# Optimization experiments

Hardware: AMD Instinct MI355X
Metric: run time of the kernel (lower is better)

The kernel has to match this reference:

```python
import jax, jax.numpy as jnp
import numpy as np

EMB = 1024
CTX = 32
F_IN, R, F_OUT = 1024, 16, 1024
N_EXP = 16
H1 = 2048   # expert / gating hidden
H2 = 512    # expert output width
B = 8


def _init(key, shape, fan_in):
    return jax.random.normal(key, shape, dtype=jnp.float32) / np.sqrt(fan_in)


def setup_inputs() -> dict:
    key = jax.random.key(0)
    ks = jax.random.split(key, 14)
    return {
        "s": jax.random.normal(ks[0], (B, EMB), dtype=jnp.float32),
        # gating: Linear(EMB,2048) -> ReLU -> Linear(2048,N_EXP) -> Softmax
        "Wg1": _init(ks[1], (EMB, H1), EMB),
        "bg1": jnp.zeros((H1,), jnp.float32),
        "Wg2": _init(ks[2], (H1, N_EXP), H1),
        "bg2": jnp.zeros((N_EXP,), jnp.float32),
        # experts (stacked): Linear(EMB+CTX,2048) -> ReLU -> Linear(2048,512)
        "W1": _init(ks[3], (N_EXP, EMB + CTX, H1), EMB + CTX),
        "b1": jnp.zeros((N_EXP, H1), jnp.float32),
        "W2": _init(ks[4], (N_EXP, H1, H2), H1),
        "b2": jnp.zeros((N_EXP, H2), jnp.float32),
        # decoders
        "WA": _init(ks[5], (H2, F_IN * R), H2),
        "bA": jnp.zeros((F_IN * R,), jnp.float32),
        "WB": _init(ks[6], (H2, R * F_OUT), H2),
        "bB": jnp.zeros((R * F_OUT,), jnp.float32),
    }


def reference(s, Wg1, bg1, Wg2, bg2, W1, b1, W2, b2, WA, bA, WB, bB):
    # gating weights over experts: [B, E]
    weights = jax.nn.softmax(jax.nn.relu(s @ Wg1 + bg1) @ Wg2 + bg2, axis=-1)

    # Expert layer-1. Input is concat([s, one_hot(c)]); since the context part
    # is a one-hot, its contribution is just a row of the context block of W1.
    W1s = W1[:, :EMB, :]              # [E, EMB, H1]
    W1c = W1[:, EMB:, :]              # [E, CTX, H1]
    base = jnp.einsum('bi,eih->ebh', s, W1s) + b1[:, None, :]   # [E, B, H1]
    # h[c,e,b,:] = relu(base[e,b,:] + W1c[e,c,:])
    h = jax.nn.relu(base[None] + jnp.transpose(W1c, (1, 0, 2))[:, :, None, :])  # [C,E,B,H1]

    # Expert layer-2: [C, E, B, H2]
    eo = jnp.einsum('cebh,ehd->cebd', h, W2) + b2[None, :, None, :]

    # softmax-weighted mixture over experts: [C, B, H2]
    z = jnp.einsum('be,cebd->cbd', weights, eo)

    A = (z @ WA + bA).reshape(CTX, B, F_IN, R)
    Bm = (z @ WB + bB).reshape(CTX, B, R, F_OUT)
    return A, Bm
```

## Files before the change

kernel.cpp:

```cpp
#include <hip/hip_runtime.h>
#include <hip/hip_bf16.h>

#define EMB 1024
#define CTX 32
#define NEXP 16
#define H1 2048
#define H2 512
#define NBIG 16384

typedef __attribute__((ext_vector_type(8))) short short8;
typedef __attribute__((ext_vector_type(4))) float floatx4;
typedef const __attribute__((address_space(1))) void* gas_t;
typedef __attribute__((address_space(3))) void* las_t;

__device__ __forceinline__ void gl16(const unsigned short* g, unsigned short* l) {
  __builtin_amdgcn_global_load_lds((gas_t)(const void*)g, (las_t)(void*)l, 16, 0, 0);
}

__device__ inline unsigned short bf_bits(float x) {
  unsigned u = __builtin_bit_cast(unsigned, x);
  u += 0x7fffu + ((u >> 16) & 1u);
  return (unsigned short)(u >> 16);
}
__device__ inline unsigned pk_bf16(float a, float b) {
  return (unsigned)bf_bits(a) | ((unsigned)bf_bits(b) << 16);
}

__global__ void __launch_bounds__(256) k_gate1(const float* __restrict__ s,
                                               const float* __restrict__ Wg1,
                                               const float* __restrict__ bg1,
                                               float* __restrict__ g1) {
  __shared__ float red[16][16][8];
  int t = threadIdx.x;
  int c = t & 15, kk = t >> 4;
  int h = blockIdx.x * 16 + c;
  float acc[8];
#pragma unroll
  for (int b = 0; b < 8; ++b) acc[b] = 0.f;
  int k0 = kk * 64;
  for (int k = k0; k < k0 + 64; ++k) {
    float w = Wg1[(size_t)k * H1 + h];
#pragma unroll
    for (int b = 0; b < 8; ++b) acc[b] += s[b * EMB + k] * w;
  }
#pragma unroll
  for (int b = 0; b < 8; ++b) red[kk][c][b] = acc[b];
  __syncthreads();
  if (t < 128) {
    int cc = t >> 3, b = t & 7;
    float v = 0.f;
#pragma unroll
    for (int q = 0; q < 16; ++q) v += red[q][cc][b];
    int hh = blockIdx.x * 16 + cc;
    v += bg1[hh];
    g1[b * H1 + hh] = fmaxf(v, 0.f);
  }
}

__global__ void __launch_bounds__(256) k_gate2(const float* __restrict__ g1,
                                               const float* __restrict__ Wg2,
                                               const float* __restrict__ bg2,
                                               float* __restrict__ logits) {
  __shared__ float red[256][8];
  int e = blockIdx.x, t = threadIdx.x;
  int k0 = t * 8;
  float wv[8];
#pragma unroll
  for (int j = 0; j < 8; ++j) wv[j] = Wg2[(size_t)(k0 + j) * NEXP + e];
  float acc[8];
#pragma unroll
  for (int b = 0; b < 8; ++b) {
    float4 ga = *(const float4*)&g1[b * H1 + k0];
    float4 gb = *(const float4*)&g1[b * H1 + k0 + 4];
    acc[b] = ga.x * wv[0] + ga.y * wv[1] + ga.z * wv[2] + ga.w * wv[3] +
             gb.x * wv[4] + gb.y * wv[5] + gb.z * wv[6] + gb.w * wv[7];
  }
#pragma unroll
  for (int b = 0; b < 8; ++b) red[t][b] = acc[b];
  __syncthreads();
  for (int off = 128; off > 0; off >>= 1) {
    if (t < off) {
#pragma unroll
      for (int b = 0; b < 8; ++b) red[t][b] += red[t + off][b];
    }
    __syncthreads();
  }
  if (t < 8) logits[t * NEXP + e] = red[0][t] + bg2[e];
}

__global__ void __launch_bounds__(512) k_base(const float* __restrict__ s,
                                              const float* __restrict__ W1,
                                              const float* __restrict__ b1,
                                              float* __restrict__ base) {
  __shared__ float sl[8 * EMB];
  __shared__ float red[8][64][17];
  int t = threadIdx.x;
  int ht = blockIdx.x;
  int e = blockIdx.y;
#pragma unroll
  for (int i = 0; i < 4; ++i) {
    int idx = (t + i * 512) * 4;
    *(float4*)&sl[idx] = *(const float4*)&s[idx];
  }
  __syncthreads();
  int hp = t & 63;
  int kk = t >> 6;
  int h = ht * 128 + hp * 2;
  const float* wp = W1 + (size_t)e * 1056 * H1 + h;
  float a0[8], a1[8];
#pragma unroll
  for (int b = 0; b < 8; ++b) { a0[b] = 0.f; a1[b] = 0.f; }
  int k0 = kk * 128;
  for (int k = k0; k < k0 + 128; ++k) {
    float2 w = *(const float2*)(wp + (size_t)k * H1);
#pragma unroll
    for (int b = 0; b < 8; ++b) {
      float sv = sl[b * EMB + k];
      a0[b] += sv * w.x;
      a1[b] += sv * w.y;
    }
  }
#pragma unroll
  for (int b = 0; b < 8; ++b) {
    red[kk][hp][b * 2] = a0[b];
    red[kk][hp][b * 2 + 1] = a1[b];
  }
  __syncthreads();
  if (t < 64) {
    int hh = ht * 128 + t * 2;
#pragma unroll
    for (int b = 0; b < 8; ++b) {
      float v0 = 0.f, v1 = 0.f;
#pragma unroll
      for (int q = 0; q < 8; ++q) {
        v0 += red[q][t][b * 2];
        v1 += red[q][t][b * 2 + 1];
      }
      float2 bv = *(const float2*)&b1[e * H1 + hh];
      float2 o;
      o.x = v0 + bv.x;
      o.y = v1 + bv.y;
      *(float2*)&base[(size_t)(e * 8 + b) * H1 + hh] = o;
    }
  }
}

__global__ void __launch_bounds__(256) k_packW(const float* __restrict__ src,
                                               unsigned short* __restrict__ dst,
                                               int Nsrc, int Ndst, int n_off,
                                               long sbs, long dbs) {
  __shared__ float tl[64][65];
  int nt = blockIdx.x, kb = blockIdx.y, bz = blockIdx.z, t = threadIdx.x;
  const float* S = src + (size_t)bz * sbs + (size_t)kb * 64 * Nsrc + nt * 64;
  int r = t >> 4, c4 = (t & 15) * 4;
#pragma unroll
  for (int i = 0; i < 4; ++i) {
    int row = r + i * 16;
    float4 v = *(const float4*)&S[(size_t)row * Nsrc + c4];
    *(float4*)&tl[row][c4] = v;
  }
  __syncthreads();
  int nl = t >> 2;
  int cb = (t & 3) * 2;
  int key = nl & 7;
  unsigned short* D = dst + (size_t)bz * dbs +
                      ((size_t)kb * Ndst + n_off + nt * 64 + nl) * 64;
#pragma unroll
  for (int j = 0; j < 2; ++j) {
    int cp = cb + j;
    int k0 = (cp ^ key) * 8;
    union { short8 v; unsigned u[4]; } p;
#pragma unroll
    for (int q = 0; q < 4; ++q)
      p.u[q] = pk_bf16(tl[k0 + 2 * q][nl], tl[k0 + 2 * q + 1][nl]);
    *(short8*)&D[cp * 8] = p.v;
  }
}

__global__ void __launch_bounds__(512) k_egemm2(const float* __restrict__ base,
                                                const float* __restrict__ W1,
                                                const unsigned short* __restrict__ W2t,
                                                float* __restrict__ eo2) {
  __shared__ __align__(16) unsigned short As[4096];
  __shared__ __align__(16) unsigned short Bs[16384];
  int id = blockIdx.x;
  int mt = id >> 6, rem = id & 63;
  int e = rem >> 2, nt = (rem >> 1) & 1, ks = rem & 1;
  int t = threadIdx.x, lane = t & 63, w = t >> 6;
  int wm = w >> 2, wn = w & 3;
  int fr = lane & 15, quad = lane >> 4, key = fr & 7;

  int am = t >> 3;
  int ak = (t & 7) * 8;
  const float* bp = base + ((size_t)e * 8 + (am & 7)) * H1;
  const float* cp = W1 + ((size_t)e * 1056 + EMB + mt * 8 + (am >> 3)) * H1;
  unsigned short* adst = &As[am * 64 + (((t & 7) ^ (am & 7)) * 8)];
  const unsigned short* wBe = W2t + (size_t)e * 1048576 + (size_t)nt * 16384;

  floatx4 zero4 = {0.f, 0.f, 0.f, 0.f};
  floatx4 acc[2][4];
#pragma unroll
  for (int i = 0; i < 2; ++i)
#pragma unroll
    for (int j = 0; j < 4; ++j) acc[i][j] = zero4;

  for (int i = 0; i < 16; ++i) {
    int kb = ks * 16 + i;
    __syncthreads();
    const unsigned short* bsrc = wBe + (size_t)kb * 32768 + t * 8;
    gl16(bsrc, &Bs[t * 8]);
    gl16(bsrc + 4096, &Bs[t * 8 + 4096]);
    gl16(bsrc + 8192, &Bs[t * 8 + 8192]);
    gl16(bsrc + 12288, &Bs[t * 8 + 12288]);
    int k0 = kb * 64 + ak;
    float4 x0 = *(const float4*)&bp[k0];
    float4 x1 = *(const float4*)&bp[k0 + 4];
    float4 y0 = *(const float4*)&cp[k0];
    float4 y1 = *(const float4*)&cp[k0 + 4];
    union { short8 v; unsigned u[4]; } pq;
    pq.u[0] = pk_bf16(fmaxf(x0.x + y0.x, 0.f), fmaxf(x0.y + y0.y, 0.f));
    pq.u[1] = pk_bf16(fmaxf(x0.z + y0.z, 0.f), fmaxf(x0.w + y0.w, 0.f));
    pq.u[2] = pk_bf16(fmaxf(x1.x + y1.x, 0.f), fmaxf(x1.y + y1.y, 0.f));
    pq.u[3] = pk_bf16(fmaxf(x1.z + y1.z, 0.f), fmaxf(x1.w + y1.w, 0.f));
    *(short8*)adst = pq.v;
    __syncthreads();
#pragma unroll
    for (int ks2 = 0; ks2 < 2; ++ks2) {
      int cof = ((ks2 * 4 + quad) ^ key) * 8;
      short8 a0 = *(const short8*)&As[(wm * 32 + fr) * 64 + cof];
      short8 a1 = *(const short8*)&As[(wm * 32 + 16 + fr) * 64 + cof];
#pragma unroll
      for (int nj = 0; nj < 4; ++nj) {
        short8 bf = *(const short8*)&Bs[(wn * 64 + nj * 16 + fr) * 64 + cof];
        acc[0][nj] = __builtin_amdgcn_mfma_f32_16x16x32_bf16(a0, bf, acc[0][nj], 0, 0, 0);
        acc[1][nj] = __builtin_amdgcn_mfma_f32_16x16x32_bf16(a1, bf, acc[1][nj], 0, 0, 0);
      }
    }
  }
  float* op = eo2 + (size_t)ks * 2097152;
  int d0 = nt * 256 + wn * 64 + fr;
#pragma unroll
  for (int nj = 0; nj < 4; ++nj) {
    int d = d0 + nj * 16;
#pragma unroll
    for (int rt = 0; rt < 2; ++rt) {
#pragma unroll
      for (int i2 = 0; i2 < 4; ++i2) {
        int gm = mt * 64 + wm * 32 + rt * 16 + quad * 4 + i2;
        op[(((size_t)(gm >> 3) * NEXP + e) * 8 + (gm & 7)) * H2 + d] = acc[rt][nj][i2];
      }
    }
  }
}

__global__ void __launch_bounds__(256) k_mix(const float* __restrict__ eo2,
                                             const float* __restrict__ logits,
                                             const float* __restrict__ b2,
                                             unsigned short* __restrict__ z_t) {
  int c = blockIdx.x, half = blockIdx.y, t = threadIdx.x;
  int b = t >> 5;
  int dc = half * 32 + (t & 31);
  int d0 = dc * 8;
  int m = c * 8 + b;
  float lg[16];
  float mx = -1e30f;
#pragma unroll
  for (int e = 0; e < 16; ++e) {
    lg[e] = logits[b * NEXP + e];
    mx = fmaxf(mx, lg[e]);
  }
  float sum = 0.f;
#pragma unroll
  for (int e = 0; e < 16; ++e) {
    lg[e] = __expf(lg[e] - mx);
    sum += lg[e];
  }
  float inv = 1.f / sum;
  float o[8];
#pragma unroll
  for (int j = 0; j < 8; ++j) o[j] = 0.f;
#pragma unroll
  for (int e = 0; e < 16; ++e) {
    float wl = lg[e] * inv;
    const float* p = &eo2[(((size_t)c * NEXP + e) * 8 + b) * H2 + d0];
    float4 x0 = *(const float4*)p;
    float4 x1 = *(const float4*)(p + 4);
    float4 y0 = *(const float4*)(p + 2097152);
    float4 y1 = *(const float4*)(p + 2097152 + 4);
    float4 v0 = *(const float4*)&b2[e * H2 + d0];
    float4 v1 = *(const float4*)&b2[e * H2 + d0 + 4];
    o[0] += wl * (x0.x + y0.x + v0.x);
    o[1] += wl * (x0.y + y0.y + v0.y);
    o[2] += wl * (x0.z + y0.z + v0.z);
    o[3] += wl * (x0.w + y0.w + v0.w);
    o[4] += wl * (x1.x + y1.x + v1.x);
    o[5] += wl * (x1.y + y1.y + v1.y);
    o[6] += wl * (x1.z + y1.z + v1.z);
    o[7] += wl * (x1.w + y1.w + v1.w);
  }
  union { short8 v; unsigned u[4]; } p;
#pragma unroll
  for (int q = 0; q < 4; ++q) p.u[q] = pk_bf16(o[2 * q], o[2 * q + 1]);
  int kb = dc >> 3;
  int cpx = (dc & 7) ^ (b & 7);
  *(short8*)&z_t[((size_t)kb * 256 + m) * 64 + cpx * 8] = p.v;
}

__global__ void __launch_bounds__(512) k_lora2(const unsigned short* __restrict__ z_t,
                                               const float* __restrict__ WA,
                                               const float* __restrict__ WB,
                                               const float* __restrict__ bA,
                                               const float* __restrict__ bB,
                                               float* __restrict__ out) {
  __shared__ __align__(16) unsigned short As[16384];
  __shared__ __align__(16) unsigned short Bs[8192];
  int nt = blockIdx.x;
  int t = threadIdx.x, lane = t & 63, w = t >> 6;
  int wm = w >> 1, wn = w & 1;
  int fr = lane & 15, quad = lane >> 4, key = fr & 7;
  int ms = nt >> 7;
  const float* Wsrc = ms ? WB : WA;
  int col0 = (nt & 127) * 128;
  int bn = t & 127, kg = t >> 7;
  const float* bw = Wsrc + col0 + bn;
  unsigned short* bd0 = &Bs[bn * 64 + (((kg * 2) ^ (bn & 7)) * 8)];
  unsigned short* bd1 = &Bs[bn * 64 + (((kg * 2 + 1) ^ (bn & 7)) * 8)];

  floatx4 zero4 = {0.f, 0.f, 0.f, 0.f};
  floatx4 acc[4][4];
#pragma unroll
  for (int i = 0; i < 4; ++i)
#pragma unroll
    for (int j = 0; j < 4; ++j) acc[i][j] = zero4;

  for (int kb = 0; kb < 8; ++kb) {
    __syncthreads();
    const unsigned short* asrc = z_t + (size_t)kb * 16384 + t * 8;
    gl16(asrc, &As[t * 8]);
    gl16(asrc + 4096, &As[t * 8 + 4096]);
    gl16(asrc + 8192, &As[t * 8 + 8192]);
    gl16(asrc + 12288, &As[t * 8 + 12288]);
    const float* bk = bw + (size_t)(kb * 64 + kg * 16) * NBIG;
    float v[16];
#pragma unroll
    for (int kr = 0; kr < 16; ++kr) v[kr] = bk[(size_t)kr * NBIG];
    union { short8 s; unsigned u[4]; } q0, q1;
#pragma unroll
    for (int q = 0; q < 4; ++q) {
      q0.u[q] = pk_bf16(v[2 * q], v[2 * q + 1]);
      q1.u[q] = pk_bf16(v[8 + 2 * q], v[9 + 2 * q]);
    }
    *(short8*)bd0 = q0.s;
    *(short8*)bd1 = q1.s;
    __syncthreads();
#pragma unroll
    for (int ks2 = 0; ks2 < 2; ++ks2) {
      int cof = ((ks2 * 4 + quad) ^ key) * 8;
      short8 bf0 = *(const short8*)&Bs[(wn * 64 + fr) * 64 + cof];
      short8 bf1 = *(const short8*)&Bs[(wn * 64 + 16 + fr) * 64 + cof];
      short8 bf2 = *(const short8*)&Bs[(wn * 64 + 32 + fr) * 64 + cof];
      short8 bf3 = *(const short8*)&Bs[(wn * 64 + 48 + fr) * 64 + cof];
#pragma unroll
      for (int rt = 0; rt < 4; ++rt) {
        short8 af = *(const short8*)&As[(wm * 64 + rt * 16 + fr) * 64 + cof];
        acc[rt][0] = __builtin_amdgcn_mfma_f32_16x16x32_bf16(af, bf0, acc[rt][0], 0, 0, 0);
        acc[rt][1] = __builtin_amdgcn_mfma_f32_16x16x32_bf16(af, bf1, acc[rt][1], 0, 0, 0);
        acc[rt][2] = __builtin_amdgcn_mfma_f32_16x16x32_bf16(af, bf2, acc[rt][2], 0, 0, 0);
        acc[rt][3] = __builtin_amdgcn_mfma_f32_16x16x32_bf16(af, bf3, acc[rt][3], 0, 0, 0);
      }
    }
  }
  const float* bias = ms ? bB : bA;
  float* obase = out + (size_t)ms * 4194304;
#pragma unroll
  for (int nj = 0; nj < 4; ++nj) {
    int nn = col0 + wn * 64 + nj * 16 + fr;
    float bv = bias[nn];
#pragma unroll
    for (int rt = 0; rt < 4; ++rt) {
#pragma unroll
      for (int i2 = 0; i2 < 4; ++i2) {
        int m = wm * 64 + rt * 16 + quad * 4 + i2;
        obase[(size_t)m * NBIG + nn] = acc[rt][nj][i2] + bv;
      }
    }
  }
}

extern "C" void kernel_launch(void* const* d_in, const int* in_sizes, int n_in,
                              void* d_out, int out_size, void* d_ws, size_t ws_size,
                              hipStream_t stream) {
  const float* s = (const float*)d_in[0];
  const float* Wg1 = (const float*)d_in[1];
  const float* bg1 = (const float*)d_in[2];
  const float* Wg2 = (const float*)d_in[3];
  const float* bg2 = (const float*)d_in[4];
  const float* W1 = (const float*)d_in[5];
  const float* b1 = (const float*)d_in[6];
  const float* W2 = (const float*)d_in[7];
  const float* b2 = (const float*)d_in[8];
  const float* WA = (const float*)d_in[9];
  const float* bA = (const float*)d_in[10];
  const float* WB = (const float*)d_in[11];
  const float* bB = (const float*)d_in[12];
  float* out = (float*)d_out;

  char* ws = (char*)d_ws;
  float* g1 = (float*)(ws);
  float* logits = (float*)(ws + 65536);
  float* base = (float*)(ws + 131072);
  float* eo2 = (float*)(ws + 1179648);
  unsigned short* z_t = (unsigned short*)(ws + 17956864);
  unsigned short* W2t = (unsigned short*)(ws + 18219008);

  k_gate1<<<128, 256, 0, stream>>>(s, Wg1, bg1, g1);
  k_gate2<<<16, 256, 0, stream>>>(g1, Wg2, bg2, logits);
  k_base<<<dim3(16, 16), 512, 0, stream>>>(s, W1, b1, base);
  k_packW<<<dim3(8, 32, 16), 256, 0, stream>>>(W2, W2t, H2, H2, 0,
                                               (long)H1 * H2, (long)H1 * H2);
  k_egemm2<<<256, 512, 0, stream>>>(base, W1, W2t, eo2);
  k_mix<<<dim3(32, 2), 256, 0, stream>>>(eo2, logits, b2, z_t);
  k_lora2<<<256, 512, 0, stream>>>(z_t, WA, WB, bA, bB, out);
}
```

Before: 390.0 us.

## Merge independent pre-stage kernels into two heterogeneous launches and widen mix grid

Gate layer 1, the expert base GEMV and the W2 bf16 repack are merged into one launch whose block ID picks the role. Gate layer 2 is folded into the expert GEMM launch as extra blocks. The mix kernel's grid is doubled with each thread handling four outputs instead of eight. This cuts launch count and lets independent work overlap on idle CUs. In exchange, the fused kernel carries a large shared allocation (about 66 KB) for every block, which may lower occupancy for the many small repack blocks.

```diff
diff --git a/kernel.cpp b/kernel.cpp
--- a/kernel.cpp
+++ b/kernel.cpp
@@ -10,6 +10,7 @@
 
 typedef __attribute__((ext_vector_type(8))) short short8;
 typedef __attribute__((ext_vector_type(4))) float floatx4;
+typedef __attribute__((ext_vector_type(2))) unsigned uint2v;
 typedef const __attribute__((address_space(1))) void* gas_t;
 typedef __attribute__((address_space(3))) void* las_t;
 
@@ -26,230 +27,230 @@
   return (unsigned)bf_bits(a) | ((unsigned)bf_bits(b) << 16);
 }
 
-__global__ void __launch_bounds__(256) k_gate1(const float* __restrict__ s,
-                                               const float* __restrict__ Wg1,
-                                               const float* __restrict__ bg1,
-                                               float* __restrict__ g1) {
-  __shared__ float red[16][16][8];
+__global__ void __launch_bounds__(512) k_fusedA(const float* __restrict__ s,
+                                                const float* __restrict__ Wg1,
+                                                const float* __restrict__ bg1,
+                                                const float* __restrict__ W1,
+                                                const float* __restrict__ b1,
+                                                const float* __restrict__ W2,
+                                                float* __restrict__ g1,
+                                                float* __restrict__ base,
+                                                unsigned short* __restrict__ W2t) {
+  __shared__ __align__(16) char smem[67584];
+  int bid = blockIdx.x;
   int t = threadIdx.x;
-  int c = t & 15, kk = t >> 4;
-  int h = blockIdx.x * 16 + c;
-  float acc[8];
-#pragma unroll
-  for (int b = 0; b < 8; ++b) acc[b] = 0.f;
-  int k0 = kk * 64;
-  for (int k = k0; k < k0 + 64; ++k) {
-    float w = Wg1[(size_t)k * H1 + h];
-#pragma unroll
-    for (int b = 0; b < 8; ++b) acc[b] += s[b * EMB + k] * w;
-  }
-#pragma unroll
-  for (int b = 0; b < 8; ++b) red[kk][c][b] = acc[b];
-  __syncthreads();
-  if (t < 128) {
-    int cc = t >> 3, b = t & 7;
-    float v = 0.f;
-#pragma unroll
-    for (int q = 0; q < 16; ++q) v += red[q][cc][b];
-    int hh = blockIdx.x * 16 + cc;
-    v += bg1[hh];
-    g1[b * H1 + hh] = fmaxf(v, 0.f);
-  }
-}
-
-__global__ void __launch_bounds__(256) k_gate2(const float* __restrict__ g1,
-                                               const float* __restrict__ Wg2,
-                                               const float* __restrict__ bg2,
-                                               float* __restrict__ logits) {
-  __shared__ float red[256][8];
-  int e = blockIdx.x, t = threadIdx.x;
-  int k0 = t * 8;
-  float wv[8];
-#pragma unroll
-  for (int j = 0; j < 8; ++j) wv[j] = Wg2[(size_t)(k0 + j) * NEXP + e];
-  float acc[8];
-#pragma unroll
-  for (int b = 0; b < 8; ++b) {
-    float4 ga = *(const float4*)&g1[b * H1 + k0];
-    float4 gb = *(const float4*)&g1[b * H1 + k0 + 4];
-    acc[b] = ga.x * wv[0] + ga.y * wv[1] + ga.z * wv[2] + ga.w * wv[3] +
-             gb.x * wv[4] + gb.y * wv[5] + gb.z * wv[6] + gb.w * wv[7];
-  }
-#pragma unroll
-  for (int b = 0; b < 8; ++b) red[t][b] = acc[b];
-  __syncthreads();
-  for (int off = 128; off > 0; off >>= 1) {
-    if (t < off) {
-#pragma unroll
-      for (int b = 0; b < 8; ++b) red[t][b] += red[t + off][b];
-    }
-    __syncthreads();
-  }
-  if (t < 8) logits[t * NEXP + e] = red[0][t] + bg2[e];
-}
-
-__global__ void __launch_bounds__(512) k_base(const float* __restrict__ s,
-                                              const float* __restrict__ W1,
-                                              const float* __restrict__ b1,
-                                              float* __restrict__ base) {
-  __shared__ float sl[8 * EMB];
-  __shared__ float red[8][64][17];
-  int t = threadIdx.x;
-  int ht = blockIdx.x;
-  int e = blockIdx.y;
-#pragma unroll
-  for (int i = 0; i < 4; ++i) {
-    int idx = (t + i * 512) * 4;
-    *(float4*)&sl[idx] = *(const float4*)&s[idx];
-  }
-  __syncthreads();
-  int hp = t & 63;
-  int kk = t >> 6;
-  int h = ht * 128 + hp * 2;
-  const float* wp = W1 + (size_t)e * 1056 * H1 + h;
-  float a0[8], a1[8];
-#pragma unroll
-  for (int b = 0; b < 8; ++b) { a0[b] = 0.f; a1[b] = 0.f; }
-  int k0 = kk * 128;
-  for (int k = k0; k < k0 + 128; ++k) {
-    float2 w = *(const float2*)(wp + (size_t)k * H1);
+
+  if (bid < 256) {
+    float* sl = (float*)smem;
+    float(*red)[64][17] = (float(*)[64][17])(smem + 32768);
+    int ht = bid & 15;
+    int e = bid >> 4;
+#pragma unroll
+    for (int i = 0; i < 4; ++i) {
+      int idx = (t + i * 512) * 4;
+      *(float4*)&sl[idx] = *(const float4*)&s[idx];
+    }
+    __syncthreads();
+    int hp = t & 63;
+    int kk = t >> 6;
+    int h = ht * 128 + hp * 2;
+    const float* wp = W1 + (size_t)e * 1056 * H1 + h;
+    float a0[8], a1[8];
+#pragma unroll
+    for (int b = 0; b < 8; ++b) { a0[b] = 0.f; a1[b] = 0.f; }
+    int k0 = kk * 128;
+    for (int k = k0; k < k0 + 128; ++k) {
+      float2 w = *(const float2*)(wp + (size_t)k * H1);
+#pragma unroll
+      for (int b = 0; b < 8; ++b) {
+        float sv = sl[b * EMB + k];
+        a0[b] += sv * w.x;
+        a1[b] += sv * w.y;
+      }
+    }
 #pragma unroll
     for (int b = 0; b < 8; ++b) {
-      float sv = sl[b * EMB + k];
-      a0[b] += sv * w.x;
-      a1[b] += sv * w.y;
-    }
-  }
-#pragma unroll
-  for (int b = 0; b < 8; ++b) {
-    red[kk][hp][b * 2] = a0[b];
-    red[kk][hp][b * 2 + 1] = a1[b];
-  }
-  __syncthreads();
-  if (t < 64) {
-    int hh = ht * 128 + t * 2;
-#pragma unroll
-    for (int b = 0; b < 8; ++b) {
-      float v0 = 0.f, v1 = 0.f;
-#pragma unroll
-      for (int q = 0; q < 8; ++q) {
-        v0 += red[q][t][b * 2];
-        v1 += red[q][t][b * 2 + 1];
-      }
-      float2 bv = *(const float2*)&b1[e * H1 + hh];
-      float2 o;
-      o.x = v0 + bv.x;
-      o.y = v1 + bv.y;
-      *(float2*)&base[(size_t)(e * 8 + b) * H1 + hh] = o;
-    }
-  }
-}
-
-__global__ void __launch_bounds__(256) k_packW(const float* __restrict__ src,
-                                               unsigned short* __restrict__ dst,
-                                               int Nsrc, int Ndst, int n_off,
-                                               long sbs, long dbs) {
-  __shared__ float tl[64][65];
-  int nt = blockIdx.x, kb = blockIdx.y, bz = blockIdx.z, t = threadIdx.x;
-  const float* S = src + (size_t)bz * sbs + (size_t)kb * 64 * Nsrc + nt * 64;
-  int r = t >> 4, c4 = (t & 15) * 4;
-#pragma unroll
-  for (int i = 0; i < 4; ++i) {
-    int row = r + i * 16;
-    float4 v = *(const float4*)&S[(size_t)row * Nsrc + c4];
-    *(float4*)&tl[row][c4] = v;
-  }
-  __syncthreads();
-  int nl = t >> 2;
-  int cb = (t & 3) * 2;
-  int key = nl & 7;
-  unsigned short* D = dst + (size_t)bz * dbs +
-                      ((size_t)kb * Ndst + n_off + nt * 64 + nl) * 64;
-#pragma unroll
-  for (int j = 0; j < 2; ++j) {
-    int cp = cb + j;
+      red[kk][hp][b * 2] = a0[b];
+      red[kk][hp][b * 2 + 1] = a1[b];
+    }
+    __syncthreads();
+    if (t < 64) {
+      int hh = ht * 128 + t * 2;
+#pragma unroll
+      for (int b = 0; b < 8; ++b) {
+        float v0 = 0.f, v1 = 0.f;
+#pragma unroll
+        for (int q = 0; q < 8; ++q) {
+          v0 += red[q][t][b * 2];
+          v1 += red[q][t][b * 2 + 1];
+        }
+        float2 bv = *(const float2*)&b1[e * H1 + hh];
+        float2 o;
+        o.x = v0 + bv.x;
+        o.y = v1 + bv.y;
+        *(float2*)&base[(size_t)(e * 8 + b) * H1 + hh] = o;
+      }
+    }
+  } else if (bid < 4352) {
+    float(*tl)[65] = (float(*)[65])smem;
+    int pid = bid - 256;
+    int nt = pid & 7, kb = (pid >> 3) & 31, e = pid >> 8;
+    const float* S = W2 + (size_t)e * H1 * H2 + (size_t)kb * 64 * H2 + nt * 64;
+    int r = t >> 4, c4 = (t & 15) * 4;
+#pragma unroll
+    for (int i = 0; i < 2; ++i) {
+      int row = r + i * 32;
+      float4 v = *(const float4*)&S[(size_t)row * H2 + c4];
+      *(float4*)&tl[row][c4] = v;
+    }
+    __syncthreads();
+    int nl = t >> 3;
+    int cp = t & 7;
+    int key = nl & 7;
+    unsigned short* D = W2t + (size_t)e * 1048576 +
+                        ((size_t)kb * 512 + nt * 64 + nl) * 64;
     int k0 = (cp ^ key) * 8;
     union { short8 v; unsigned u[4]; } p;
 #pragma unroll
     for (int q = 0; q < 4; ++q)
       p.u[q] = pk_bf16(tl[k0 + 2 * q][nl], tl[k0 + 2 * q + 1][nl]);
     *(short8*)&D[cp * 8] = p.v;
-  }
-}
-
-__global__ void __launch_bounds__(512) k_egemm2(const float* __restrict__ base,
+  } else {
+    float(*red1)[16][8] = (float(*)[16][8])smem;
+    int gid = bid - 4352;
+    int c = t & 15, kk = t >> 4;
+    int h = gid * 16 + c;
+    float acc[8];
+#pragma unroll
+    for (int b = 0; b < 8; ++b) acc[b] = 0.f;
+    int k0 = kk * 32;
+    for (int k = k0; k < k0 + 32; ++k) {
+      float w = Wg1[(size_t)k * H1 + h];
+#pragma unroll
+      for (int b = 0; b < 8; ++b) acc[b] += s[b * EMB + k] * w;
+    }
+#pragma unroll
+    for (int b = 0; b < 8; ++b) red1[kk][c][b] = acc[b];
+    __syncthreads();
+    if (t < 128) {
+      int cc = t >> 3, b = t & 7;
+      float v = 0.f;
+#pragma unroll
+      for (int q = 0; q < 32; ++q) v += red1[q][cc][b];
+      int hh = gid * 16 + cc;
+      v += bg1[hh];
+      g1[b * H1 + hh] = fmaxf(v, 0.f);
+    }
+  }
+}
+
+__global__ void __launch_bounds__(512) k_fusedB(const float* __restrict__ base,
                                                 const float* __restrict__ W1,
                                                 const unsigned short* __restrict__ W2t,
-                                                float* __restrict__ eo2) {
-  __shared__ __align__(16) unsigned short As[4096];
-  __shared__ __align__(16) unsigned short Bs[16384];
-  int id = blockIdx.x;
-  int mt = id >> 6, rem = id & 63;
-  int e = rem >> 2, nt = (rem >> 1) & 1, ks = rem & 1;
-  int t = threadIdx.x, lane = t & 63, w = t >> 6;
-  int wm = w >> 2, wn = w & 3;
-  int fr = lane & 15, quad = lane >> 4, key = fr & 7;
-
-  int am = t >> 3;
-  int ak = (t & 7) * 8;
-  const float* bp = base + ((size_t)e * 8 + (am & 7)) * H1;
-  const float* cp = W1 + ((size_t)e * 1056 + EMB + mt * 8 + (am >> 3)) * H1;
-  unsigned short* adst = &As[am * 64 + (((t & 7) ^ (am & 7)) * 8)];
-  const unsigned short* wBe = W2t + (size_t)e * 1048576 + (size_t)nt * 16384;
-
-  floatx4 zero4 = {0.f, 0.f, 0.f, 0.f};
-  floatx4 acc[2][4];
-#pragma unroll
-  for (int i = 0; i < 2; ++i)
-#pragma unroll
-    for (int j = 0; j < 4; ++j) acc[i][j] = zero4;
-
-  for (int i = 0; i < 16; ++i) {
-    int kb = ks * 16 + i;
-    __syncthreads();
-    const unsigned short* bsrc = wBe + (size_t)kb * 32768 + t * 8;
-    gl16(bsrc, &Bs[t * 8]);
-    gl16(bsrc + 4096, &Bs[t * 8 + 4096]);
-    gl16(bsrc + 8192, &Bs[t * 8 + 8192]);
-    gl16(bsrc + 12288, &Bs[t * 8 + 12288]);
-    int k0 = kb * 64 + ak;
-    float4 x0 = *(const float4*)&bp[k0];
-    float4 x1 = *(const float4*)&bp[k0 + 4];
-    float4 y0 = *(const float4*)&cp[k0];
-    float4 y1 = *(const float4*)&cp[k0 + 4];
-    union { short8 v; unsigned u[4]; } pq;
-    pq.u[0] = pk_bf16(fmaxf(x0.x + y0.x, 0.f), fmaxf(x0.y + y0.y, 0.f));
-    pq.u[1] = pk_bf16(fmaxf(x0.z + y0.z, 0.f), fmaxf(x0.w + y0.w, 0.f));
-    pq.u[2] = pk_bf16(fmaxf(x1.x + y1.x, 0.f), fmaxf(x1.y + y1.y, 0.f));
-    pq.u[3] = pk_bf16(fmaxf(x1.z + y1.z, 0.f), fmaxf(x1.w + y1.w, 0.f));
-    *(short8*)adst = pq.v;
-    __syncthreads();
-#pragma unroll
-    for (int ks2 = 0; ks2 < 2; ++ks2) {
-      int cof = ((ks2 * 4 + quad) ^ key) * 8;
-      short8 a0 = *(const short8*)&As[(wm * 32 + fr) * 64 + cof];
-      short8 a1 = *(const short8*)&As[(wm * 32 + 16 + fr) * 64 + cof];
-#pragma unroll
-      for (int nj = 0; nj < 4; ++nj) {
-        short8 bf = *(const short8*)&Bs[(wn * 64 + nj * 16 + fr) * 64 + cof];
-        acc[0][nj] = __builtin_amdgcn_mfma_f32_16x16x32_bf16(a0, bf, acc[0][nj], 0, 0, 0);
-        acc[1][nj] = __builtin_amdgcn_mfma_f32_16x16x32_bf16(a1, bf, acc[1][nj], 0, 0, 0);
-      }
-    }
-  }
-  float* op = eo2 + (size_t)ks * 2097152;
-  int d0 = nt * 256 + wn * 64 + fr;
-#pragma unroll
-  for (int nj = 0; nj < 4; ++nj) {
-    int d = d0 + nj * 16;
-#pragma unroll
-    for (int rt = 0; rt < 2; ++rt) {
-#pragma unroll
-      for (int i2 = 0; i2 < 4; ++i2) {
-        int gm = mt * 64 + wm * 32 + rt * 16 + quad * 4 + i2;
-        op[(((size_t)(gm >> 3) * NEXP + e) * 8 + (gm & 7)) * H2 + d] = acc[rt][nj][i2];
-      }
-    }
+                                                const float* __restrict__ g1,
+                                                const float* __restrict__ Wg2,
+                                                const float* __restrict__ bg2,
+                                                float* __restrict__ eo2,
+                                                float* __restrict__ logits) {
+  __shared__ __align__(16) char smemB[40960];
+  int bid = blockIdx.x;
+  int t = threadIdx.x;
+
+  if (bid < 256) {
+    unsigned short* As = (unsigned short*)smemB;
+    unsigned short* Bs = (unsigned short*)(smemB + 8192);
+    int id = bid;
+    int mt = id >> 6, rem = id & 63;
+    int e = rem >> 2, nt = (rem >> 1) & 1, ks = rem & 1;
+    int lane = t & 63, w = t >> 6;
+    int wm = w >> 2, wn = w & 3;
+    int fr = lane & 15, quad = lane >> 4, key = fr & 7;
+
+    int am = t >> 3;
+    int ak = (t & 7) * 8;
+    const float* bp = base + ((size_t)e * 8 + (am & 7)) * H1;
+    const float* cp = W1 + ((size_t)e * 1056 + EMB + mt * 8 + (am >> 3)) * H1;
+    unsigned short* adst = &As[am * 64 + (((t & 7) ^ (am & 7)) * 8)];
+    const unsigned short* wBe = W2t + (size_t)e * 1048576 + (size_t)nt * 16384;
+
+    floatx4 zero4 = {0.f, 0.f, 0.f, 0.f};
+    floatx4 acc[2][4];
+#pragma unroll
+    for (int i = 0; i < 2; ++i)
+#pragma unroll
+      for (int j = 0; j < 4; ++j) acc[i][j] = zero4;
+
+    for (int i = 0; i < 16; ++i) {
+      int kb = ks * 16 + i;
+      __syncthreads();
+      const unsigned short* bsrc = wBe + (size_t)kb * 32768 + t * 8;
+      gl16(bsrc, &Bs[t * 8]);
+      gl16(bsrc + 4096, &Bs[t * 8 + 4096]);
+      gl16(bsrc + 8192, &Bs[t * 8 + 8192]);
+      gl16(bsrc + 12288, &Bs[t * 8 + 12288]);
+      int k0 = kb * 64 + ak;
+      float4 x0 = *(const float4*)&bp[k0];
+      float4 x1 = *(const float4*)&bp[k0 + 4];
+      float4 y0 = *(const float4*)&cp[k0];
+      float4 y1 = *(const float4*)&cp[k0 + 4];
+      union { short8 v; unsigned u[4]; } pq;
+      pq.u[0] = pk_bf16(fmaxf(x0.x + y0.x, 0.f), fmaxf(x0.y + y0.y, 0.f));
+      pq.u[1] = pk_bf16(fmaxf(x0.z + y0.z, 0.f), fmaxf(x0.w + y0.w, 0.f));
+      pq.u[2] = pk_bf16(fmaxf(x1.x + y1.x, 0.f), fmaxf(x1.y + y1.y, 0.f));
+      pq.u[3] = pk_bf16(fmaxf(x1.z + y1.z, 0.f), fmaxf(x1.w + y1.w, 0.f));
+      *(short8*)adst = pq.v;
+      __syncthreads();
+#pragma unroll
+      for (int ks2 = 0; ks2 < 2; ++ks2) {
+        int cof = ((ks2 * 4 + quad) ^ key) * 8;
+        short8 a0 = *(const short8*)&As[(wm * 32 + fr) * 64 + cof];
+        short8 a1 = *(const short8*)&As[(wm * 32 + 16 + fr) * 64 + cof];
+#pragma unroll
+        for (int nj = 0; nj < 4; ++nj) {
+          short8 bf = *(const short8*)&Bs[(wn * 64 + nj * 16 + fr) * 64 + cof];
+          acc[0][nj] = __builtin_amdgcn_mfma_f32_16x16x32_bf16(a0, bf, acc[0][nj], 0, 0, 0);
+          acc[1][nj] = __builtin_amdgcn_mfma_f32_16x16x32_bf16(a1, bf, acc[1][nj], 0, 0, 0);
+        }
+      }
+    }
+    float* op = eo2 + (size_t)ks * 2097152;
+    int d0 = nt * 256 + wn * 64 + fr;
+#pragma unroll
+    for (int nj = 0; nj < 4; ++nj) {
+      int d = d0 + nj * 16;
+#pragma unroll
+      for (int rt = 0; rt < 2; ++rt) {
+#pragma unroll
+        for (int i2 = 0; i2 < 4; ++i2) {
+          int gm = mt * 64 + wm * 32 + rt * 16 + quad * 4 + i2;
+          op[(((size_t)(gm >> 3) * NEXP + e) * 8 + (gm & 7)) * H2 + d] = acc[rt][nj][i2];
+        }
+      }
+    }
+  } else {
+    float(*red)[8] = (float(*)[8])smemB;
+    int e = bid - 256;
+    int k0 = t * 4;
+    float wv[4];
+#pragma unroll
+    for (int j = 0; j < 4; ++j) wv[j] = Wg2[(size_t)(k0 + j) * NEXP + e];
+    float acc[8];
+#pragma unroll
+    for (int b = 0; b < 8; ++b) {
+      float4 ga = *(const float4*)&g1[b * H1 + k0];
+      acc[b] = ga.x * wv[0] + ga.y * wv[1] + ga.z * wv[2] + ga.w * wv[3];
+    }
+#pragma unroll
+    for (int b = 0; b < 8; ++b) red[t][b] = acc[b];
+    __syncthreads();
+    for (int off = 256; off > 0; off >>= 1) {
+      if (t < off) {
+#pragma unroll
+        for (int b = 0; b < 8; ++b) red[t][b] += red[t + off][b];
+      }
+      __syncthreads();
+    }
+    if (t < 8) logits[t * NEXP + e] = red[0][t] + bg2[e];
   }
 }
 
@@ -257,10 +258,12 @@
                                              const float* __restrict__ logits,
                                              const float* __restrict__ b2,
                                              unsigned short* __restrict__ z_t) {
-  int c = blockIdx.x, half = blockIdx.y, t = threadIdx.x;
+  int c = blockIdx.x, by = blockIdx.y, t = threadIdx.x;
   int b = t >> 5;
-  int dc = half * 32 + (t & 31);
-  int d0 = dc * 8;
+  int x = t & 31;
+  int dc = by * 16 + (x >> 1);
+  int part = x & 1;
+  int d0 = dc * 8 + part * 4;
   int m = c * 8 + b;
   float lg[16];
   float mx = -1e30f;
@@ -276,34 +279,27 @@
     sum += lg[e];
   }
   float inv = 1.f / sum;
-  float o[8];
-#pragma unroll
-  for (int j = 0; j < 8; ++j) o[j] = 0.f;
+  float o[4];
+#pragma unroll
+  for (int j = 0; j < 4; ++j) o[j] = 0.f;
 #pragma unroll
   for (int e = 0; e < 16; ++e) {
     float wl = lg[e] * inv;
     const float* p = &eo2[(((size_t)c * NEXP + e) * 8 + b) * H2 + d0];
     float4 x0 = *(const float4*)p;
-    float4 x1 = *(const float4*)(p + 4);
     float4 y0 = *(const float4*)(p + 2097152);
-    float4 y1 = *(const float4*)(p + 2097152 + 4);
     float4 v0 = *(const float4*)&b2[e * H2 + d0];
-    float4 v1 = *(const float4*)&b2[e * H2 + d0 + 4];
     o[0] += wl * (x0.x + y0.x + v0.x);
     o[1] += wl * (x0.y + y0.y + v0.y);
     o[2] += wl * (x0.z + y0.z + v0.z);
     o[3] += wl * (x0.w + y0.w + v0.w);
-    o[4] += wl * (x1.x + y1.x + v1.x);
-    o[5] += wl * (x1.y + y1.y + v1.y);
-    o[6] += wl * (x1.z + y1.z + v1.z);
-    o[7] += wl * (x1.w + y1.w + v1.w);
-  }
-  union { short8 v; unsigned u[4]; } p;
-#pragma unroll
-  for (int q = 0; q < 4; ++q) p.u[q] = pk_bf16(o[2 * q], o[2 * q + 1]);
+  }
+  uint2v p;
+  p.x = pk_bf16(o[0], o[1]);
+  p.y = pk_bf16(o[2], o[3]);
   int kb = dc >> 3;
   int cpx = (dc & 7) ^ (b & 7);
-  *(short8*)&z_t[((size_t)kb * 256 + m) * 64 + cpx * 8] = p.v;
+  *(uint2v*)&z_t[((size_t)kb * 256 + m) * 64 + cpx * 8 + part * 4] = p;
 }
 
 __global__ void __launch_bounds__(512) k_lora2(const unsigned short* __restrict__ z_t,
@@ -413,12 +409,8 @@
   unsigned short* z_t = (unsigned short*)(ws + 17956864);
   unsigned short* W2t = (unsigned short*)(ws + 18219008);
 
-  k_gate1<<<128, 256, 0, stream>>>(s, Wg1, bg1, g1);
-  k_gate2<<<16, 256, 0, stream>>>(g1, Wg2, bg2, logits);
-  k_base<<<dim3(16, 16), 512, 0, stream>>>(s, W1, b1, base);
-  k_packW<<<dim3(8, 32, 16), 256, 0, stream>>>(W2, W2t, H2, H2, 0,
-                                               (long)H1 * H2, (long)H1 * H2);
-  k_egemm2<<<256, 512, 0, stream>>>(base, W1, W2t, eo2);
-  k_mix<<<dim3(32, 2), 256, 0, stream>>>(eo2, logits, b2, z_t);
+  k_fusedA<<<4480, 512, 0, stream>>>(s, Wg1, bg1, W1, b1, W2, g1, base, W2t);
+  k_fusedB<<<272, 512, 0, stream>>>(base, W1, W2t, g1, Wg2, bg2, eo2, logits);
+  k_mix<<<dim3(32, 4), 256, 0, stream>>>(eo2, logits, b2, z_t);
   k_lora2<<<256, 512, 0, stream>>>(z_t, WA, WB, bA, bB, out);
 }
```

Result: faster. 376.7 us (-3.4%).
